# Performance work log

Measured on AMD Instinct MI355X. Metric: run time of the kernel, lower is better.

The kernel has to match this reference:

```python
import jax, jax.numpy as jnp
import numpy as np

K = 5            # trend_kernel_size
PAD = K // 2
EPS = 1e-5

def _ricker(k):
    # Ricker (mexican-hat) wavelet used as the Peaks kernel
    a = k / 4.0
    t = np.arange(k, dtype=np.float64) - (k - 1) / 2.0
    A = 2.0 / (np.sqrt(3.0 * a) * np.pi ** 0.25)
    return (A * (1.0 - (t / a) ** 2) * np.exp(-t ** 2 / (2.0 * a ** 2))).astype(np.float32)

def _ramp(k):
    # centered linear ramp -> local slope estimator for the Trend kernel
    return (np.linspace(-1.0, 1.0, k) / k).astype(np.float32)

_PEAK_W = jnp.asarray(_ricker(K))
_RAMP_W = jnp.asarray(_ramp(K))

def tconv(x, w):
    # 'same'-padded cross-correlation along the time axis (axis=2) of (B,C,T,H,W)
    T = x.shape[2]
    xp = jnp.pad(x, ((0, 0), (0, 0), (PAD, PAD), (0, 0), (0, 0)))
    out = w[0] * jax.lax.dynamic_slice_in_dim(xp, 0, T, axis=2)
    for j in range(1, K):
        out = out + w[j] * jax.lax.dynamic_slice_in_dim(xp, j, T, axis=2)
    return out

def bn(x, gamma, beta, axes):
    # training-mode batch norm over `axes`, channel axis = 1
    m = x.mean(axes, keepdims=True)
    v = x.var(axes, keepdims=True)
    xn = (x - m) * jax.lax.rsqrt(v + EPS)
    shp = [1] * x.ndim
    shp[1] = -1
    return xn * gamma.reshape(shp) + beta.reshape(shp)


def setup_inputs() -> dict:
    key = jax.random.key(0)
    ks = jax.random.split(key, 8)
    B, C, T, H, W = 4, 3, 12, 256, 256
    CH0 = 32
    return {
        'x':      jax.random.normal(ks[0], (B, C, T, H, W), jnp.float32),
        'w0':     jax.random.normal(ks[1], (CH0, C), jnp.float32) * 0.1,
        'g0':     jnp.ones((CH0,), jnp.float32),
        'b0':     jnp.zeros((CH0,), jnp.float32),
        'wrt':    jax.random.normal(ks[2], (1, CH0), jnp.float32) * 0.1,
        'grt':    jnp.ones((1,), jnp.float32),
        'brt':    jnp.zeros((1,), jnp.float32),
        'wtt':    jax.random.normal(ks[3], (1, C), jnp.float32) * 0.1,
        'gtt':    jnp.ones((1,), jnp.float32),
        'btt':    jnp.zeros((1,), jnp.float32),
        'w_th':   jax.random.normal(ks[4], (CH0, T), jnp.float32) * 0.1,
        'b_th':   jnp.zeros((CH0,), jnp.float32),
        'g_min':  jnp.ones((CH0,), jnp.float32),
        'b_min':  jnp.zeros((CH0,), jnp.float32),
        'g_max':  jnp.ones((CH0,), jnp.float32),
        'b_max':  jnp.zeros((CH0,), jnp.float32),
        'g_mean': jnp.ones((CH0,), jnp.float32),
        'b_mean': jnp.zeros((CH0,), jnp.float32),
    }


def reference(x, w0, g0, b0, wrt, grt, brt, wtt, gtt, btt,
              w_th, b_th, g_min, b_min, g_max, b_max, g_mean, b_mean):
    act = jax.nn.silu
    # --- per-band temporal kernels (vectorized over all bands/pixels) ---
    peak = tconv(x, _PEAK_W)                       # Peaks: ricker wavelet
    slope = tconv(x, _RAMP_W)                      # Trend: local slope
    trend = peak + jax.nn.relu(slope) + jax.nn.relu(-slope)  # (B,C,T,H,W)
    # --- time_conv0: 1x1x1 conv3d + BN3d + act ---
    h = act(bn(jnp.einsum('bcthw,oc->bothw', x, w0), g0, b0, (0, 2, 3, 4)))  # (B,32,T,H,W)
    # --- reduce_to_time / reduce_trend_to_time: 1x1x1 conv3d to 1 channel ---
    rt = act(bn(jnp.einsum('bcthw,oc->bothw', h, wrt), grt, brt, (0, 2, 3, 4)))[:, 0]      # (B,T,H,W)
    tt = act(bn(jnp.einsum('bcthw,oc->bothw', trend, wtt), gtt, btt, (0, 2, 3, 4)))[:, 0]  # (B,T,H,W)
    # --- time_to_hidden: 1x1 conv2d over the time-as-channels axis ---
    time_logits = jnp.einsum('bthw,ot->bohw', rt + tt, w_th) + b_th[None, :, None, None]
    # --- channel reductions over time + BN2d + act (mean branch uses max, as in source) ---
    xmin = h.min(axis=2)
    xmax = h.max(axis=2)
    cmin = act(bn(xmin, g_min, b_min, (0, 2, 3)))
    cmax = act(bn(xmax, g_max, b_max, (0, 2, 3)))
    cmean = act(bn(xmax, g_mean, b_mean, (0, 2, 3)))
    enc = time_logits + cmin + cmax + cmean        # (B,32,H,W)
    # --- InstanceNorm2d(affine=False) ---
    m = enc.mean((2, 3), keepdims=True)
    v = enc.var((2, 3), keepdims=True)
    return (enc - m) * jax.lax.rsqrt(v + EPS)
```

## Files before the change

kernel.cpp:

```cpp
#include <hip/hip_runtime.h>
#include <math.h>

#define HW_    65536
#define THW_   786432
#define NP     262144
#define N1_    3145728.0
#define N3_    262144.0

#define XB 0
#define SB 512
#define RB 1536
#define EB 1792
#define DWN 2816

__device__ __constant__ float PW_[5] = {-0.33647654f, 0.20279402f, 0.77575913f, 0.20279402f, -0.33647654f};
__device__ __constant__ float RW_[5] = {-0.2f, -0.1f, 0.0f, 0.1f, 0.2f};

typedef __fp16 fp16x2 __attribute__((ext_vector_type(2)));
union H2U { fp16x2 h; unsigned int u; };
__device__ __forceinline__ unsigned int packh(float a, float b) {
  H2U x; x.h = __builtin_amdgcn_cvt_pkrtz(a, b); return x.u;
}
__device__ __forceinline__ float2 unpackh(unsigned int v) {
  H2U x; x.u = v; return make_float2((float)x.h.x, (float)x.h.y);
}
__device__ __forceinline__ unsigned short pack1h(float a) {
  return (unsigned short)(packh(a, 0.f) & 0xffffu);
}

__device__ __forceinline__ float wred64(float v) {
#pragma unroll
  for (int m = 32; m > 0; m >>= 1) v += __shfl_xor(v, m, 64);
  return v;
}

__device__ __forceinline__ float fsilu(float y) {
  float e = __expf(-y);
  return y * __builtin_amdgcn_rcpf(1.0f + e);
}

__global__ __launch_bounds__(256) void k_xstats(const float* __restrict__ x, double* __restrict__ dws) {
  const int bb = blockIdx.x & 1;
  const int v = (blockIdx.x >> 1) * 256 + threadIdx.x;
  const float4* x4 = (const float4*)x;
  float s0 = 0, s1 = 0, s2 = 0, p00 = 0, p01 = 0, p02 = 0, p11 = 0, p12 = 0, p22 = 0;
#pragma unroll
  for (int bi = 0; bi < 2; bi++) {
    int b = bb * 2 + bi;
    float4 a0 = x4[(size_t)(b * 3 + 0) * 196608 + v];
    float4 a1 = x4[(size_t)(b * 3 + 1) * 196608 + v];
    float4 a2 = x4[(size_t)(b * 3 + 2) * 196608 + v];
    s0 += a0.x + a0.y + a0.z + a0.w;
    s1 += a1.x + a1.y + a1.z + a1.w;
    s2 += a2.x + a2.y + a2.z + a2.w;
    p00 += a0.x * a0.x + a0.y * a0.y + a0.z * a0.z + a0.w * a0.w;
    p11 += a1.x * a1.x + a1.y * a1.y + a1.z * a1.z + a1.w * a1.w;
    p22 += a2.x * a2.x + a2.y * a2.y + a2.z * a2.z + a2.w * a2.w;
    p01 += a0.x * a1.x + a0.y * a1.y + a0.z * a1.z + a0.w * a1.w;
    p02 += a0.x * a2.x + a0.y * a2.y + a0.z * a2.z + a0.w * a2.w;
    p12 += a1.x * a2.x + a1.y * a2.y + a1.z * a2.z + a1.w * a2.w;
  }
  float vals[9] = {s0, s1, s2, p00, p01, p02, p11, p12, p22};
  __shared__ float red[4][9];
  int wave = threadIdx.x >> 6, lane = threadIdx.x & 63;
#pragma unroll
  for (int q = 0; q < 9; q++) vals[q] = wred64(vals[q]);
  if (lane == 0) {
#pragma unroll
    for (int q = 0; q < 9; q++) red[wave][q] = vals[q];
  }
  __syncthreads();
  if (threadIdx.x < 9) {
    double t = (double)red[0][threadIdx.x] + red[1][threadIdx.x] + red[2][threadIdx.x] + red[3][threadIdx.x];
    atomicAdd(&dws[XB + (blockIdx.x & 31) * 16 + threadIdx.x], t);
  }
}

__global__ void k_fin0(const double* __restrict__ dws, const float* __restrict__ w0,
                       const float* __restrict__ g0, const float* __restrict__ b0,
                       float* __restrict__ cf) {
  int o = threadIdx.x;
  if (o >= 32) return;
  double q[9];
#pragma unroll
  for (int i = 0; i < 9; i++) {
    double t = 0;
#pragma unroll
    for (int s = 0; s < 32; s++) t += dws[XB + s * 16 + i];
    q[i] = t / N1_;
  }
  double c0 = w0[o * 3 + 0], c1 = w0[o * 3 + 1], c2 = w0[o * 3 + 2];
  double Ey = c0 * q[0] + c1 * q[1] + c2 * q[2];
  double Ey2 = c0 * c0 * q[3] + c1 * c1 * q[6] + c2 * c2 * q[8] +
               2.0 * (c0 * c1 * q[4] + c0 * c2 * q[5] + c1 * c2 * q[7]);
  double var = Ey2 - Ey * Ey;
  double alpha = (double)g0[o] / sqrt(var + 1e-5);
  cf[o]      = (float)(alpha * c0);
  cf[32 + o] = (float)(alpha * c1);
  cf[64 + o] = (float)(alpha * c2);
  cf[96 + o] = (float)((double)b0[o] - Ey * alpha);
}

__global__ __launch_bounds__(256) void k_passB(const float* __restrict__ x, const float* __restrict__ wrt,
                                               const float* __restrict__ wtt, const float* __restrict__ cf,
                                               unsigned int* __restrict__ pRT, unsigned int* __restrict__ pMM,
                                               double* __restrict__ dws) {
  const int tid = threadIdx.x;
  const int pix = blockIdx.x * 256 + tid;
  const int b = pix >> 16, hw = pix & 65535;
  __shared__ float red[4][4];
  __shared__ float cfa0[32], cfa1[32], cfa2[32], cfb[32];
  if (tid < 32) {
    cfa0[tid] = cf[tid];
    cfa1[tid] = cf[32 + tid];
    cfa2[tid] = cf[64 + tid];
    cfb[tid]  = cf[96 + tid];
  }
  __syncthreads();

  const float* xp = x + (size_t)b * 3 * THW_ + hw;
  float xv[3][12];
#pragma unroll
  for (int c = 0; c < 3; c++)
#pragma unroll
    for (int t = 0; t < 12; t++) xv[c][t] = xp[(size_t)(c * 12 + t) * HW_];
  float wt[3] = {wtt[0], wtt[1], wtt[2]};
  float ttp[12];
#pragma unroll
  for (int t = 0; t < 12; t++) {
    float acc = 0.f;
#pragma unroll
    for (int c = 0; c < 3; c++) {
      float pk = 0.f, sl = 0.f;
#pragma unroll
      for (int j = 0; j < 5; j++) {
        int tj = t - 2 + j;
        if (tj >= 0 && tj < 12) {
          pk = fmaf(PW_[j], xv[c][tj], pk);
          sl = fmaf(RW_[j], xv[c][tj], sl);
        }
      }
      acc = fmaf(wt[c], pk + fabsf(sl), acc);
    }
    ttp[t] = acc;
  }
  float rt_t[12];
#pragma unroll
  for (int t = 0; t < 12; t++) rt_t[t] = 0.f;
#pragma unroll
  for (int o = 0; o < 32; o++) {
    float a0 = cfa0[o], a1 = cfa1[o], a2 = cfa2[o];
    float bet = cfb[o], wo = wrt[o];
    float mn = 3.4e38f, mx = -3.4e38f;
#pragma unroll
    for (int t = 0; t < 12; t++) {
      float y = fmaf(a0, xv[0][t], fmaf(a1, xv[1][t], fmaf(a2, xv[2][t], bet)));
      float h = fsilu(y);
      mn = fminf(mn, h);
      mx = fmaxf(mx, h);
      rt_t[t] = fmaf(wo, h, rt_t[t]);
    }
    pMM[o * NP + pix] = packh(mn, mx);
  }
#pragma unroll
  for (int t = 0; t < 12; t++) pRT[t * NP + pix] = packh(rt_t[t], ttp[t]);

  {
    float srt = 0.f, ssrt = 0.f, stt = 0.f, sstt = 0.f;
#pragma unroll
    for (int t = 0; t < 12; t++) {
      srt += rt_t[t];  ssrt = fmaf(rt_t[t], rt_t[t], ssrt);
      stt += ttp[t];   sstt = fmaf(ttp[t], ttp[t], sstt);
    }
    srt = wred64(srt); ssrt = wred64(ssrt); stt = wred64(stt); sstt = wred64(sstt);
    int wave = tid >> 6, lane = tid & 63;
    if (lane == 0) { red[wave][0] = srt; red[wave][1] = ssrt; red[wave][2] = stt; red[wave][3] = sstt; }
  }
  __syncthreads();
  if (tid < 4) {
    double v = (double)red[0][tid] + red[1][tid] + red[2][tid] + red[3][tid];
    atomicAdd(&dws[RB + (blockIdx.x & 31) * 8 + tid], v);
  }
}

__global__ __launch_bounds__(256) void k_stats(const unsigned int* __restrict__ pMM,
                                               double* __restrict__ dws) {
  __shared__ float red[4][4];
  int o = blockIdx.x >> 5, sub = blockIdx.x & 31, tid = threadIdx.x;
  const uint4* p = (const uint4*)(pMM + (size_t)o * NP);
  int base = sub * 256 + tid;
  float s0 = 0, s1 = 0, s2 = 0, s3 = 0;
#pragma unroll
  for (int it = 0; it < 8; it++) {
    uint4 v = p[base + it * 8192];
    float2 a = unpackh(v.x), b = unpackh(v.y), c = unpackh(v.z), d = unpackh(v.w);
    s0 += a.x + b.x + c.x + d.x;
    s1 += a.x * a.x + b.x * b.x + c.x * c.x + d.x * d.x;
    s2 += a.y + b.y + c.y + d.y;
    s3 += a.y * a.y + b.y * b.y + c.y * c.y + d.y * d.y;
  }
  s0 = wred64(s0); s1 = wred64(s1); s2 = wred64(s2); s3 = wred64(s3);
  int wave = tid >> 6, lane = tid & 63;
  if (lane == 0) { red[wave][0] = s0; red[wave][1] = s1; red[wave][2] = s2; red[wave][3] = s3; }
  __syncthreads();
  if (tid < 4) {
    double v = (double)red[0][tid] + red[1][tid] + red[2][tid] + red[3][tid];
    atomicAdd(&dws[SB + (o * 4 + tid) * 8 + (blockIdx.x & 7)], v);
  }
}

template<bool FP16OUT>
__global__ __launch_bounds__(256) void k_passC(const unsigned int* __restrict__ pRT,
                                               const unsigned int* __restrict__ pMM,
                                               const float* __restrict__ wth, const float* __restrict__ bth,
                                               const float* __restrict__ grt, const float* __restrict__ brt,
                                               const float* __restrict__ gtt, const float* __restrict__ btt,
                                               const float* __restrict__ gmin, const float* __restrict__ bmin,
                                               const float* __restrict__ gmax, const float* __restrict__ bmax,
                                               const float* __restrict__ gmean, const float* __restrict__ bmean,
                                               const double* __restrict__ dws, float* __restrict__ out,
                                               unsigned short* __restrict__ penc) {
  const int tid = threadIdx.x;
  const int pix = blockIdx.x * 256 + tid;
  const int b = pix >> 16, hw = pix & 65535;
  __shared__ float camn[32], cbmn[32], camx[32], cbmx[32], came[32], cbme[32];
  __shared__ float c4[4];

  if (tid < 32) {
    double q[4];
#pragma unroll
    for (int i = 0; i < 4; i++) {
      double t = 0;
#pragma unroll
      for (int s = 0; s < 8; s++) t += dws[SB + (tid * 4 + i) * 8 + s];
      q[i] = t / N3_;
    }
    double m = q[0], v = q[1] - m * m;
    double a = (double)gmin[tid] / sqrt(v + 1e-5);
    camn[tid] = (float)a; cbmn[tid] = (float)((double)bmin[tid] - m * a);
    double mm = q[2], vv = q[3] - mm * mm;
    a = (double)gmax[tid] / sqrt(vv + 1e-5);
    camx[tid] = (float)a; cbmx[tid] = (float)((double)bmax[tid] - mm * a);
    a = (double)gmean[tid] / sqrt(vv + 1e-5);
    came[tid] = (float)a; cbme[tid] = (float)((double)bmean[tid] - mm * a);
  }
  if (tid == 32) {
    double q[4];
#pragma unroll
    for (int i = 0; i < 4; i++) {
      double t = 0;
#pragma unroll
      for (int s = 0; s < 32; s++) t += dws[RB + s * 8 + i];
      q[i] = t / N1_;
    }
    double m = q[0], v = q[1] - m * m;
    double a = (double)grt[0] / sqrt(v + 1e-5);
    c4[0] = (float)a; c4[1] = (float)((double)brt[0] - m * a);
    m = q[2]; v = q[3] - m * m;
    a = (double)gtt[0] / sqrt(v + 1e-5);
    c4[2] = (float)a; c4[3] = (float)((double)btt[0] - m * a);
  }
  __syncthreads();

  float art = c4[0], brt_ = c4[1], att = c4[2], btt_ = c4[3];
  float rtt[12];
#pragma unroll
  for (int t = 0; t < 12; t++) {
    float2 v = unpackh(pRT[t * NP + pix]);
    rtt[t] = fsilu(fmaf(art, v.x, brt_)) + fsilu(fmaf(att, v.y, btt_));
  }
  float* po = out + (size_t)b * 32 * HW_ + hw;
  unsigned short* pe = penc + ((size_t)(b * 32) << 16) + hw;
#pragma unroll
  for (int o = 0; o < 32; o++) {
    float2 mm = unpackh(pMM[o * NP + pix]);
    float tl = bth[o];
#pragma unroll
    for (int t = 0; t < 12; t++) tl = fmaf(wth[o * 12 + t], rtt[t], tl);
    float e = tl + fsilu(fmaf(camn[o], mm.x, cbmn[o]))
                 + fsilu(fmaf(camx[o], mm.y, cbmx[o]))
                 + fsilu(fmaf(came[o], mm.y, cbme[o]));
    if (FP16OUT) pe[(size_t)o << 16] = pack1h(e);
    else         po[(size_t)o * HW_] = e;
  }
}

__global__ __launch_bounds__(256) void k_encstats16(const unsigned short* __restrict__ penc,
                                                    double* __restrict__ dws) {
  __shared__ float red[4][2];
  int s = blockIdx.x >> 2, sub = blockIdx.x & 3, tid = threadIdx.x;
  const uint4* p = (const uint4*)(penc + ((size_t)s << 16));
  float S = 0, SS = 0;
#pragma unroll
  for (int it = 0; it < 8; it++) {
    uint4 v = p[sub * 2048 + tid + it * 256];
    float2 a = unpackh(v.x), b = unpackh(v.y), c = unpackh(v.z), d = unpackh(v.w);
    S += a.x + a.y + b.x + b.y + c.x + c.y + d.x + d.y;
    SS += a.x * a.x + a.y * a.y + b.x * b.x + b.y * b.y +
          c.x * c.x + c.y * c.y + d.x * d.x + d.y * d.y;
  }
  S = wred64(S); SS = wred64(SS);
  int wave = tid >> 6, lane = tid & 63;
  if (lane == 0) { red[wave][0] = S; red[wave][1] = SS; }
  __syncthreads();
  if (tid < 2) {
    double v = (double)red[0][tid] + red[1][tid] + red[2][tid] + red[3][tid];
    atomicAdd(&dws[EB + (s * 2 + tid) * 4 + sub], v);
  }
}

__global__ __launch_bounds__(256) void k_inorm16(const double* __restrict__ dws,
                                                 const unsigned short* __restrict__ penc,
                                                 float* __restrict__ out) {
  int s = blockIdx.y;
  double S = 0, SS = 0;
#pragma unroll
  for (int sh = 0; sh < 4; sh++) {
    S  += dws[EB + (s * 2 + 0) * 4 + sh];
    SS += dws[EB + (s * 2 + 1) * 4 + sh];
  }
  double m = S / 65536.0, v = SS / 65536.0 - m * m;
  float rstd = (float)(1.0 / sqrt(v + 1e-5));
  float mf = (float)m;
  const uint2* p = (const uint2*)(penc + ((size_t)s << 16));
  float4* po = (float4*)(out + ((size_t)s << 16));
  int i = blockIdx.x * 256 + threadIdx.x;
  uint2 u = p[i];
  float2 a = unpackh(u.x), b = unpackh(u.y);
  float4 r;
  r.x = (a.x - mf) * rstd;
  r.y = (a.y - mf) * rstd;
  r.z = (b.x - mf) * rstd;
  r.w = (b.y - mf) * rstd;
  po[i] = r;
}

__global__ __launch_bounds__(256) void k_encstats32(const float* __restrict__ out, double* __restrict__ dws) {
  __shared__ float red[4][2];
  int s = blockIdx.x >> 2, sub = blockIdx.x & 3, tid = threadIdx.x;
  const float4* p = (const float4*)(out + ((size_t)s << 16));
  float S = 0, SS = 0;
#pragma unroll 4
  for (int it = 0; it < 16; it++) {
    float4 a = p[sub * 256 + tid + it * 1024];
    S += a.x + a.y + a.z + a.w;
    SS += a.x * a.x + a.y * a.y + a.z * a.z + a.w * a.w;
  }
  S = wred64(S); SS = wred64(SS);
  int wave = tid >> 6, lane = tid & 63;
  if (lane == 0) { red[wave][0] = S; red[wave][1] = SS; }
  __syncthreads();
  if (tid < 2) {
    double v = (double)red[0][tid] + red[1][tid] + red[2][tid] + red[3][tid];
    atomicAdd(&dws[EB + (s * 2 + tid) * 4 + sub], v);
  }
}

__global__ __launch_bounds__(256) void k_inorm32(const double* __restrict__ dws, float* __restrict__ out) {
  int s = blockIdx.y;
  double S = 0, SS = 0;
#pragma unroll
  for (int sh = 0; sh < 4; sh++) {
    S  += dws[EB + (s * 2 + 0) * 4 + sh];
    SS += dws[EB + (s * 2 + 1) * 4 + sh];
  }
  double m = S / 65536.0, v = SS / 65536.0 - m * m;
  float rstd = (float)(1.0 / sqrt(v + 1e-5));
  float mf = (float)m;
  float4* p = (float4*)(out + ((size_t)s << 16));
  int i = blockIdx.x * 256 + threadIdx.x;
  float4 a = p[i];
  a.x = (a.x - mf) * rstd;
  a.y = (a.y - mf) * rstd;
  a.z = (a.z - mf) * rstd;
  a.w = (a.w - mf) * rstd;
  p[i] = a;
}

extern "C" void kernel_launch(void* const* d_in, const int* in_sizes, int n_in,
                              void* d_out, int out_size, void* d_ws, size_t ws_size,
                              hipStream_t stream) {
  const float* x     = (const float*)d_in[0];
  const float* w0    = (const float*)d_in[1];
  const float* g0    = (const float*)d_in[2];
  const float* b0    = (const float*)d_in[3];
  const float* wrt   = (const float*)d_in[4];
  const float* grt   = (const float*)d_in[5];
  const float* brt   = (const float*)d_in[6];
  const float* wtt   = (const float*)d_in[7];
  const float* gtt   = (const float*)d_in[8];
  const float* btt   = (const float*)d_in[9];
  const float* wth   = (const float*)d_in[10];
  const float* bth   = (const float*)d_in[11];
  const float* gmin  = (const float*)d_in[12];
  const float* bmin  = (const float*)d_in[13];
  const float* gmax  = (const float*)d_in[14];
  const float* bmax  = (const float*)d_in[15];
  const float* gmean = (const float*)d_in[16];
  const float* bmean = (const float*)d_in[17];
  double* dws = (double*)d_ws;
  float* cf = (float*)((char*)d_ws + 32768);
  unsigned int* pRT = (unsigned int*)((char*)d_ws + 65536);
  unsigned int* pMM = pRT + 12 * NP;
  unsigned short* pENC = (unsigned short*)(pMM + 32 * NP);
  const size_t need16 = 65536 + (size_t)12 * NP * 4 + (size_t)32 * NP * 4 + (size_t)32 * NP * 2;
  const bool big = ws_size >= need16;
  float* out = (float*)d_out;

  hipMemsetAsync(d_ws, 0, DWN * sizeof(double), stream);
  hipLaunchKernelGGL(k_xstats, dim3(1536), dim3(256), 0, stream, x, dws);
  hipLaunchKernelGGL(k_fin0, dim3(1), dim3(32), 0, stream, dws, w0, g0, b0, cf);
  hipLaunchKernelGGL(k_passB, dim3(1024), dim3(256), 0, stream, x, wrt, wtt, cf, pRT, pMM, dws);
  hipLaunchKernelGGL(k_stats, dim3(1024), dim3(256), 0, stream, pMM, dws);
  if (big) {
    hipLaunchKernelGGL((k_passC<true>), dim3(1024), dim3(256), 0, stream, pRT, pMM, wth, bth,
                       grt, brt, gtt, btt, gmin, bmin, gmax, bmax, gmean, bmean, dws, out, pENC);
    hipLaunchKernelGGL(k_encstats16, dim3(512), dim3(256), 0, stream, pENC, dws);
    hipLaunchKernelGGL(k_inorm16, dim3(64, 128), dim3(256), 0, stream, dws, pENC, out);
  } else {
    hipLaunchKernelGGL((k_passC<false>), dim3(1024), dim3(256), 0, stream, pRT, pMM, wth, bth,
                       grt, brt, gtt, btt, gmin, bmin, gmax, bmax, gmean, bmean, dws, out, pENC);
    hipLaunchKernelGGL(k_encstats32, dim3(512), dim3(256), 0, stream, out, dws);
    hipLaunchKernelGGL(k_inorm32, dim3(64, 128), dim3(256), 0, stream, dws, out);
  }
}
```

Measured before the change: 104.4 us.

## Fuse BN0 finalize into xstats and encoder stats into passC

```diff
diff --git a/kernel.cpp b/kernel.cpp
--- a/kernel.cpp
+++ b/kernel.cpp
@@ -39,7 +39,16 @@
   return y * __builtin_amdgcn_rcpf(1.0f + e);
 }
 
-__global__ __launch_bounds__(256) void k_xstats(const float* __restrict__ x, double* __restrict__ dws) {
+__device__ __forceinline__ double aload(const double* p) {
+  return __hip_atomic_load(p, __ATOMIC_RELAXED, __HIP_MEMORY_SCOPE_AGENT);
+}
+
+__global__ __launch_bounds__(256) void k_xstats(const float* __restrict__ x,
+                                                const float* __restrict__ w0,
+                                                const float* __restrict__ g0,
+                                                const float* __restrict__ b0,
+                                                float* __restrict__ cf,
+                                                double* __restrict__ dws) {
   const int bb = blockIdx.x & 1;
   const int v = (blockIdx.x >> 1) * 256 + threadIdx.x;
   const float4* x4 = (const float4*)x;
@@ -62,6 +71,7 @@
   }
   float vals[9] = {s0, s1, s2, p00, p01, p02, p11, p12, p22};
   __shared__ float red[4][9];
+  __shared__ unsigned int isLast;
   int wave = threadIdx.x >> 6, lane = threadIdx.x & 63;
 #pragma unroll
   for (int q = 0; q < 9; q++) vals[q] = wred64(vals[q]);
@@ -74,31 +84,35 @@
     double t = (double)red[0][threadIdx.x] + red[1][threadIdx.x] + red[2][threadIdx.x] + red[3][threadIdx.x];
     atomicAdd(&dws[XB + (blockIdx.x & 31) * 16 + threadIdx.x], t);
   }
-}
-
-__global__ void k_fin0(const double* __restrict__ dws, const float* __restrict__ w0,
-                       const float* __restrict__ g0, const float* __restrict__ b0,
-                       float* __restrict__ cf) {
-  int o = threadIdx.x;
-  if (o >= 32) return;
-  double q[9];
-#pragma unroll
-  for (int i = 0; i < 9; i++) {
-    double t = 0;
-#pragma unroll
-    for (int s = 0; s < 32; s++) t += dws[XB + s * 16 + i];
-    q[i] = t / N1_;
-  }
-  double c0 = w0[o * 3 + 0], c1 = w0[o * 3 + 1], c2 = w0[o * 3 + 2];
-  double Ey = c0 * q[0] + c1 * q[1] + c2 * q[2];
-  double Ey2 = c0 * c0 * q[3] + c1 * c1 * q[6] + c2 * c2 * q[8] +
-               2.0 * (c0 * c1 * q[4] + c0 * c2 * q[5] + c1 * c2 * q[7]);
-  double var = Ey2 - Ey * Ey;
-  double alpha = (double)g0[o] / sqrt(var + 1e-5);
-  cf[o]      = (float)(alpha * c0);
-  cf[32 + o] = (float)(alpha * c1);
-  cf[64 + o] = (float)(alpha * c2);
-  cf[96 + o] = (float)((double)b0[o] - Ey * alpha);
+  __syncthreads();
+  if (threadIdx.x == 0) {
+    __threadfence();
+    unsigned int* cnt = (unsigned int*)(dws + DWN);
+    unsigned int vv = __hip_atomic_fetch_add(cnt, 1u, __ATOMIC_ACQ_REL, __HIP_MEMORY_SCOPE_AGENT);
+    isLast = (vv == 1535u);
+  }
+  __syncthreads();
+  if (isLast && threadIdx.x < 32) {
+    int o = threadIdx.x;
+    double q[9];
+#pragma unroll
+    for (int i = 0; i < 9; i++) {
+      double t = 0;
+#pragma unroll
+      for (int s = 0; s < 32; s++) t += aload(&dws[XB + s * 16 + i]);
+      q[i] = t / N1_;
+    }
+    double c0 = w0[o * 3 + 0], c1 = w0[o * 3 + 1], c2 = w0[o * 3 + 2];
+    double Ey = c0 * q[0] + c1 * q[1] + c2 * q[2];
+    double Ey2 = c0 * c0 * q[3] + c1 * c1 * q[6] + c2 * c2 * q[8] +
+                 2.0 * (c0 * c1 * q[4] + c0 * c2 * q[5] + c1 * c2 * q[7]);
+    double var = Ey2 - Ey * Ey;
+    double alpha = (double)g0[o] / sqrt(var + 1e-5);
+    cf[o]      = (float)(alpha * c0);
+    cf[32 + o] = (float)(alpha * c1);
+    cf[64 + o] = (float)(alpha * c2);
+    cf[96 + o] = (float)((double)b0[o] - Ey * alpha);
+  }
 }
 
 __global__ __launch_bounds__(256) void k_passB(const float* __restrict__ x, const float* __restrict__ wrt,
@@ -218,13 +232,14 @@
                                                const float* __restrict__ gmin, const float* __restrict__ bmin,
                                                const float* __restrict__ gmax, const float* __restrict__ bmax,
                                                const float* __restrict__ gmean, const float* __restrict__ bmean,
-                                               const double* __restrict__ dws, float* __restrict__ out,
+                                               double* __restrict__ dws, float* __restrict__ out,
                                                unsigned short* __restrict__ penc) {
   const int tid = threadIdx.x;
   const int pix = blockIdx.x * 256 + tid;
   const int b = pix >> 16, hw = pix & 65535;
   __shared__ float camn[32], cbmn[32], camx[32], cbmx[32], came[32], cbme[32];
   __shared__ float c4[4];
+  __shared__ float lenc[32 * 264];
 
   if (tid < 32) {
     double q[4];
@@ -269,8 +284,6 @@
     float2 v = unpackh(pRT[t * NP + pix]);
     rtt[t] = fsilu(fmaf(art, v.x, brt_)) + fsilu(fmaf(att, v.y, btt_));
   }
-  float* po = out + (size_t)b * 32 * HW_ + hw;
-  unsigned short* pe = penc + ((size_t)(b * 32) << 16) + hw;
 #pragma unroll
   for (int o = 0; o < 32; o++) {
     float2 mm = unpackh(pMM[o * NP + pix]);
@@ -280,32 +293,35 @@
     float e = tl + fsilu(fmaf(camn[o], mm.x, cbmn[o]))
                  + fsilu(fmaf(camx[o], mm.y, cbmx[o]))
                  + fsilu(fmaf(came[o], mm.y, cbme[o]));
+    lenc[o * 264 + tid] = e;
+  }
+  __syncthreads();
+  {
+    int o = tid >> 3, j = tid & 7;
+    float s = 0, s2 = 0;
+#pragma unroll
+    for (int k = 0; k < 32; k++) {
+      float e = lenc[o * 264 + j + k * 8];
+      s += e; s2 = fmaf(e, e, s2);
+    }
+#pragma unroll
+    for (int m = 1; m < 8; m <<= 1) {
+      s  += __shfl_xor(s, m, 64);
+      s2 += __shfl_xor(s2, m, 64);
+    }
+    if (j == 0) {
+      int sh = blockIdx.x & 3;
+      atomicAdd(&dws[EB + ((b * 32 + o) * 2 + 0) * 4 + sh], (double)s);
+      atomicAdd(&dws[EB + ((b * 32 + o) * 2 + 1) * 4 + sh], (double)s2);
+    }
+  }
+  float* po = out + (size_t)b * 32 * HW_ + hw;
+  unsigned short* pe = penc + ((size_t)(b * 32) << 16) + hw;
+#pragma unroll
+  for (int o = 0; o < 32; o++) {
+    float e = lenc[o * 264 + tid];
     if (FP16OUT) pe[(size_t)o << 16] = pack1h(e);
     else         po[(size_t)o * HW_] = e;
-  }
-}
-
-__global__ __launch_bounds__(256) void k_encstats16(const unsigned short* __restrict__ penc,
-                                                    double* __restrict__ dws) {
-  __shared__ float red[4][2];
-  int s = blockIdx.x >> 2, sub = blockIdx.x & 3, tid = threadIdx.x;
-  const uint4* p = (const uint4*)(penc + ((size_t)s << 16));
-  float S = 0, SS = 0;
-#pragma unroll
-  for (int it = 0; it < 8; it++) {
-    uint4 v = p[sub * 2048 + tid + it * 256];
-    float2 a = unpackh(v.x), b = unpackh(v.y), c = unpackh(v.z), d = unpackh(v.w);
-    S += a.x + a.y + b.x + b.y + c.x + c.y + d.x + d.y;
-    SS += a.x * a.x + a.y * a.y + b.x * b.x + b.y * b.y +
-          c.x * c.x + c.y * c.y + d.x * d.x + d.y * d.y;
-  }
-  S = wred64(S); SS = wred64(SS);
-  int wave = tid >> 6, lane = tid & 63;
-  if (lane == 0) { red[wave][0] = S; red[wave][1] = SS; }
-  __syncthreads();
-  if (tid < 2) {
-    double v = (double)red[0][tid] + red[1][tid] + red[2][tid] + red[3][tid];
-    atomicAdd(&dws[EB + (s * 2 + tid) * 4 + sub], v);
   }
 }
 
@@ -333,27 +349,6 @@
   r.z = (b.x - mf) * rstd;
   r.w = (b.y - mf) * rstd;
   po[i] = r;
-}
-
-__global__ __launch_bounds__(256) void k_encstats32(const float* __restrict__ out, double* __restrict__ dws) {
-  __shared__ float red[4][2];
-  int s = blockIdx.x >> 2, sub = blockIdx.x & 3, tid = threadIdx.x;
-  const float4* p = (const float4*)(out + ((size_t)s << 16));
-  float S = 0, SS = 0;
-#pragma unroll 4
-  for (int it = 0; it < 16; it++) {
-    float4 a = p[sub * 256 + tid + it * 1024];
-    S += a.x + a.y + a.z + a.w;
-    SS += a.x * a.x + a.y * a.y + a.z * a.z + a.w * a.w;
-  }
-  S = wred64(S); SS = wred64(SS);
-  int wave = tid >> 6, lane = tid & 63;
-  if (lane == 0) { red[wave][0] = S; red[wave][1] = SS; }
-  __syncthreads();
-  if (tid < 2) {
-    double v = (double)red[0][tid] + red[1][tid] + red[2][tid] + red[3][tid];
-    atomicAdd(&dws[EB + (s * 2 + tid) * 4 + sub], v);
-  }
 }
 
 __global__ __launch_bounds__(256) void k_inorm32(const double* __restrict__ dws, float* __restrict__ out) {
@@ -407,20 +402,17 @@
   const bool big = ws_size >= need16;
   float* out = (float*)d_out;
 
-  hipMemsetAsync(d_ws, 0, DWN * sizeof(double), stream);
-  hipLaunchKernelGGL(k_xstats, dim3(1536), dim3(256), 0, stream, x, dws);
-  hipLaunchKernelGGL(k_fin0, dim3(1), dim3(32), 0, stream, dws, w0, g0, b0, cf);
+  hipMemsetAsync(d_ws, 0, DWN * sizeof(double) + 64, stream);
+  hipLaunchKernelGGL(k_xstats, dim3(1536), dim3(256), 0, stream, x, w0, g0, b0, cf, dws);
   hipLaunchKernelGGL(k_passB, dim3(1024), dim3(256), 0, stream, x, wrt, wtt, cf, pRT, pMM, dws);
   hipLaunchKernelGGL(k_stats, dim3(1024), dim3(256), 0, stream, pMM, dws);
   if (big) {
     hipLaunchKernelGGL((k_passC<true>), dim3(1024), dim3(256), 0, stream, pRT, pMM, wth, bth,
                        grt, brt, gtt, btt, gmin, bmin, gmax, bmax, gmean, bmean, dws, out, pENC);
-    hipLaunchKernelGGL(k_encstats16, dim3(512), dim3(256), 0, stream, pENC, dws);
     hipLaunchKernelGGL(k_inorm16, dim3(64, 128), dim3(256), 0, stream, dws, pENC, out);
   } else {
     hipLaunchKernelGGL((k_passC<false>), dim3(1024), dim3(256), 0, stream, pRT, pMM, wth, bth,
                        grt, brt, gtt, btt, gmin, bmin, gmax, bmax, gmean, bmean, dws, out, pENC);
-    hipLaunchKernelGGL(k_encstats32, dim3(512), dim3(256), 0, stream, out, dws);
     hipLaunchKernelGGL(k_inorm32, dim3(64, 128), dim3(256), 0, stream, dws, out);
   }
 }
```

Result: slower. 171.6 us (+64.3%).
